# Kernel tuning notes

Hardware: AMD Instinct MI355X
Metric: run time of the kernel (lower is better)

The kernel has to match this reference:

```python
import jax, jax.numpy as jnp
import numpy as np

D_MODEL = 1024
NUM_HEADS = 16
HEAD_DIM = D_MODEL // NUM_HEADS  # 64
SEQ = 2048
BATCH = 4
LN_EPS = 1e-5


def setup_inputs() -> dict:
    key = jax.random.key(0)
    k_in, k_qkv, k_o, k_g = jax.random.split(key, 4)
    inputs = jax.random.normal(k_in, (BATCH, SEQ, D_MODEL), dtype=jnp.float32)
    mask = jnp.zeros((BATCH, 1, SEQ, SEQ), dtype=jnp.float32)  # additive mask
    # Realistic rotary embeddings (RoPE), duplicated-halves layout
    inv_freq = 1.0 / (10000.0 ** (jnp.arange(0, HEAD_DIM, 2, dtype=jnp.float32) / HEAD_DIM))
    pos = jnp.arange(SEQ, dtype=jnp.float32)
    freqs = pos[:, None] * inv_freq[None, :]            # [S, Dh/2]
    emb = jnp.concatenate([freqs, freqs], axis=-1)       # [S, Dh]
    cos = jnp.cos(emb)
    sin = jnp.sin(emb)
    # Parameters
    sd = 1.0 / np.sqrt(D_MODEL)
    w_qkv = jax.random.normal(k_qkv, (D_MODEL, 3 * D_MODEL), dtype=jnp.float32) * sd
    w_o = jax.random.normal(k_o, (D_MODEL, D_MODEL), dtype=jnp.float32) * sd
    ln_gamma = jnp.ones((D_MODEL,), dtype=jnp.float32)
    return {"inputs": inputs, "mask": mask, "cos": cos, "sin": sin,
            "ln_gamma": ln_gamma, "w_qkv": w_qkv, "w_o": w_o}


def _rotate_half(x):
    x1, x2 = jnp.split(x, 2, axis=-1)
    return jnp.concatenate([-x2, x1], axis=-1)


def reference(inputs, mask, cos, sin, ln_gamma, w_qkv, w_o):
    B, S, D = inputs.shape
    # Pre-attention LayerNorm (layer_id != 0), center=False -> no beta
    mu = jnp.mean(inputs, axis=-1, keepdims=True)
    var = jnp.mean(jnp.square(inputs - mu), axis=-1, keepdims=True)
    x = (inputs - mu) / jnp.sqrt(var + LN_EPS) * ln_gamma
    # Fused QKV projection, split into heads: [B, H, S, Dh]
    qkv = (x @ w_qkv).reshape(B, S, 3, NUM_HEADS, HEAD_DIM)
    qkv = jnp.transpose(qkv, (2, 0, 3, 1, 4))
    q, k, v = qkv[0], qkv[1], qkv[2]
    # RoPE
    c = cos.reshape(1, 1, S, HEAD_DIM)
    s = sin.reshape(1, 1, S, HEAD_DIM)
    q = q * c + _rotate_half(q) * s
    k = k * c + _rotate_half(k) * s
    # Scaled dot-product attention with additive mask
    scale = 1.0 / jnp.sqrt(jnp.asarray(HEAD_DIM, dtype=q.dtype))
    logits = jnp.einsum("bhqd,bhkd->bhqk", q, k) * scale + mask
    attn = jax.nn.softmax(logits, axis=-1)
    out = jnp.einsum("bhqk,bhkd->bhqd", attn, v)
    out = jnp.transpose(out, (0, 2, 1, 3)).reshape(B, S, D)
    return out @ w_o
```

## Files before the change

### kernel.cpp

```cpp
#include <hip/hip_runtime.h>
#include <stdint.h>

#define DEV __device__ __forceinline__

typedef __bf16 bf16x8 __attribute__((ext_vector_type(8)));
typedef float f32x4 __attribute__((ext_vector_type(4)));
typedef float f32x16 __attribute__((ext_vector_type(16)));

DEV unsigned short f2bf(float f) {
  union { float f; uint32_t u; } c; c.f = f;
  uint32_t u = c.u;
  u += 0x7FFFu + ((u >> 16) & 1u);
  return (unsigned short)(u >> 16);
}
DEV float bf2f(unsigned short h) {
  union { uint32_t u; float f; } c; c.u = ((uint32_t)h) << 16;
  return c.f;
}
DEV float u2f(uint32_t u) {
  union { uint32_t u; float f; } c; c.u = u;
  return c.f;
}
DEV bf16x8 ld8(const unsigned short* p) {
  uint4 u = *reinterpret_cast<const uint4*>(p);
  return __builtin_bit_cast(bf16x8, u);
}
DEV uint32_t cvtpk(float lo, float hi) {
  uint32_t r;
  asm("v_cvt_pk_bf16_f32 %0, %1, %2" : "=v"(r) : "v"(lo), "v"(hi));
  return r;
}
DEV void permswap(uint32_t& a, uint32_t& b) {
  asm("v_permlane32_swap_b32 %0, %1" : "+v"(a), "+v"(b));
}
DEV float exp2b(float x) { return __builtin_amdgcn_exp2f(x); }
DEV void gload16(const void* g, void* l) {
  __builtin_amdgcn_global_load_lds((const __attribute__((address_space(1))) void*)g,
                                   (__attribute__((address_space(3))) void*)l, 16, 0, 0);
}

template<int K, int N>
__global__ __launch_bounds__(256)
void transpose_cast_kernel(const float* __restrict__ in, unsigned short* __restrict__ out) {
  __shared__ float tile[64][65];
  const int bk = blockIdx.x % (K / 64);
  const int bn = blockIdx.x / (K / 64);
  const int k0 = bk * 64, n0 = bn * 64;
  const int t = threadIdx.x;
#pragma unroll
  for (int i = 0; i < 16; ++i) {
    int idx = t + i * 256;
    int kl = idx >> 6, nl = idx & 63;
    tile[kl][nl] = in[(size_t)(k0 + kl) * N + n0 + nl];
  }
  __syncthreads();
#pragma unroll
  for (int i = 0; i < 16; ++i) {
    int idx = t + i * 256;
    int nl = idx >> 6, kl = idx & 63;
    out[(size_t)(n0 + nl) * K + k0 + kl] = f2bf(tile[kl][nl]);
  }
}

__global__ __launch_bounds__(256)
void ln_kernel(const float* __restrict__ x, const float* __restrict__ gamma,
               unsigned short* __restrict__ y) {
  const int row = blockIdx.x;
  const int t = threadIdx.x;
  const float4 v = reinterpret_cast<const float4*>(x + (size_t)row * 1024)[t];
  float s  = v.x + v.y + v.z + v.w;
  float s2 = v.x * v.x + v.y * v.y + v.z * v.z + v.w * v.w;
#pragma unroll
  for (int off = 1; off < 64; off <<= 1) {
    s  += __shfl_xor(s, off);
    s2 += __shfl_xor(s2, off);
  }
  __shared__ float red[8];
  const int w = t >> 6, lane = t & 63;
  if (lane == 0) { red[w] = s; red[4 + w] = s2; }
  __syncthreads();
  s  = red[0] + red[1] + red[2] + red[3];
  s2 = red[4] + red[5] + red[6] + red[7];
  const float mu = s * (1.0f / 1024.0f);
  const float var = s2 * (1.0f / 1024.0f) - mu * mu;
  const float rstd = rsqrtf(var + 1e-5f);
  const float4 g = reinterpret_cast<const float4*>(gamma)[t];
  ushort4 o;
  o.x = f2bf((v.x - mu) * rstd * g.x);
  o.y = f2bf((v.y - mu) * rstd * g.y);
  o.z = f2bf((v.z - mu) * rstd * g.z);
  o.w = f2bf((v.w - mu) * rstd * g.w);
  reinterpret_cast<ushort4*>(y + (size_t)row * 1024)[t] = o;
}

template<int N_DIM>
__global__ __launch_bounds__(256)
void gemm_bt_kernel(const unsigned short* __restrict__ A,
                    const unsigned short* __restrict__ Bt,
                    float* __restrict__ Cout) {
  constexpr int K = 1024;
  __shared__ unsigned short a_lds[128 * 32];
  __shared__ unsigned short b_lds[128 * 32];
  const int t = threadIdx.x;
  const int w = t >> 6, l = t & 63;
  const int lrow = l & 15, lch = l >> 4;
  const int nbn = N_DIM / 128;
  const int m0 = (blockIdx.x / nbn) * 128;
  const int n0 = (blockIdx.x % nbn) * 128;
  const int wm = (w >> 1) * 64, wn = (w & 1) * 64;

  const int srow = t >> 2;
  const int schk = t & 3;
  const int scol = ((schk ^ (srow & 3)) << 3);
  const unsigned short* aS0 = A  + (size_t)(m0 + srow) * K + scol;
  const unsigned short* aS1 = A  + (size_t)(m0 + 64 + srow) * K + scol;
  const unsigned short* bS0 = Bt + (size_t)(n0 + srow) * K + scol;
  const unsigned short* bS1 = Bt + (size_t)(n0 + 64 + srow) * K + scol;
  unsigned short* aD0 = a_lds + (w * 16) * 32;
  unsigned short* aD1 = a_lds + (64 + w * 16) * 32;
  unsigned short* bD0 = b_lds + (w * 16) * 32;
  unsigned short* bD1 = b_lds + (64 + w * 16) * 32;

  f32x4 acc[4][4] = {};

  for (int k0 = 0; k0 < K; k0 += 32) {
    gload16(aS0 + k0, aD0);
    gload16(aS1 + k0, aD1);
    gload16(bS0 + k0, bD0);
    gload16(bS1 + k0, bD1);
    __syncthreads();
    bf16x8 af[4], bfr[4];
#pragma unroll
    for (int m = 0; m < 4; ++m) {
      int row = wm + m * 16 + lrow;
      af[m] = ld8(a_lds + row * 32 + ((lch ^ (lrow & 3)) << 3));
    }
#pragma unroll
    for (int n = 0; n < 4; ++n) {
      int row = wn + n * 16 + lrow;
      bfr[n] = ld8(b_lds + row * 32 + ((lch ^ (lrow & 3)) << 3));
    }
#pragma unroll
    for (int m = 0; m < 4; ++m)
#pragma unroll
      for (int n = 0; n < 4; ++n)
        acc[m][n] = __builtin_amdgcn_mfma_f32_16x16x32_bf16(af[m], bfr[n], acc[m][n], 0, 0, 0);
    __syncthreads();
  }

#pragma unroll
  for (int m = 0; m < 4; ++m) {
    const int grow0 = m0 + wm + m * 16 + lch * 4;
#pragma unroll
    for (int n = 0; n < 4; ++n) {
      const int gcol = n0 + wn + n * 16 + lrow;
#pragma unroll
      for (int r = 0; r < 4; ++r)
        Cout[(size_t)(grow0 + r) * N_DIM + gcol] = acc[m][n][r];
    }
  }
}

__global__ __launch_bounds__(256)
void gemm_qkv_rope_kernel(const unsigned short* __restrict__ A,
                          const unsigned short* __restrict__ Bt,
                          const float* __restrict__ cosb,
                          const float* __restrict__ sinb,
                          unsigned short* __restrict__ Qo,
                          unsigned short* __restrict__ Ko,
                          unsigned short* __restrict__ Vo) {
  constexpr int K = 1024;
  constexpr int N_DIM = 3072;
  __shared__ unsigned short a_lds[128 * 32];
  __shared__ unsigned short b_lds[128 * 32];
  const int t = threadIdx.x;
  const int w = t >> 6, l = t & 63;
  const int lrow = l & 15, lch = l >> 4;
  const int nbn = N_DIM / 128;
  const int m0 = (blockIdx.x / nbn) * 128;
  const int n0 = (blockIdx.x % nbn) * 128;
  const int wm = (w >> 1) * 64, wn = (w & 1) * 64;

  const int srow = t >> 2;
  const int schk = t & 3;
  const int scol = ((schk ^ (srow & 3)) << 3);
  const unsigned short* aS0 = A  + (size_t)(m0 + srow) * K + scol;
  const unsigned short* aS1 = A  + (size_t)(m0 + 64 + srow) * K + scol;
  const unsigned short* bS0 = Bt + (size_t)(n0 + srow) * K + scol;
  const unsigned short* bS1 = Bt + (size_t)(n0 + 64 + srow) * K + scol;
  unsigned short* aD0 = a_lds + (w * 16) * 32;
  unsigned short* aD1 = a_lds + (64 + w * 16) * 32;
  unsigned short* bD0 = b_lds + (w * 16) * 32;
  unsigned short* bD1 = b_lds + (64 + w * 16) * 32;

  f32x4 acc[4][4] = {};

  for (int k0 = 0; k0 < K; k0 += 32) {
    gload16(aS0 + k0, aD0);
    gload16(aS1 + k0, aD1);
    gload16(bS0 + k0, bD0);
    gload16(bS1 + k0, bD1);
    __syncthreads();
    bf16x8 af[4], bfr[4];
#pragma unroll
    for (int m = 0; m < 4; ++m) {
      int row = wm + m * 16 + lrow;
      af[m] = ld8(a_lds + row * 32 + ((lch ^ (lrow & 3)) << 3));
    }
#pragma unroll
    for (int n = 0; n < 4; ++n) {
      int row = wn + n * 16 + lrow;
      bfr[n] = ld8(b_lds + row * 32 + ((lch ^ (lrow & 3)) << 3));
    }
#pragma unroll
    for (int m = 0; m < 4; ++m)
#pragma unroll
      for (int n = 0; n < 4; ++n)
        acc[m][n] = __builtin_amdgcn_mfma_f32_16x16x32_bf16(af[m], bfr[n], acc[m][n], 0, 0, 0);
    __syncthreads();
  }

  const int b = m0 >> 11;
  const int sbase = (m0 & 2047) + wm;
  const int region = n0 >> 10;
  const int h = ((n0 & 1023) >> 6) + (w & 1);

  if (region < 2) {
    const float qs = (region == 0) ? 0.180336880f : 1.0f;
    unsigned short* dst = (region == 0 ? Qo : Ko) + (size_t)(b * 16 + h) * 2048 * 64;
#pragma unroll
    for (int m = 0; m < 4; ++m) {
#pragma unroll
      for (int r = 0; r < 4; ++r) {
        const int sg = sbase + m * 16 + lch * 4 + r;
        const float* crow = cosb + (size_t)sg * 64;
        const float* srow2 = sinb + (size_t)sg * 64;
        unsigned short* drow = dst + (size_t)sg * 64;
#pragma unroll
        for (int np = 0; np < 2; ++np) {
          const int d0 = np * 16 + lrow;
          const int d1 = d0 + 32;
          const float v0 = acc[m][np][r];
          const float v1 = acc[m][np + 2][r];
          const float r0 = v0 * crow[d0] - v1 * srow2[d0];
          const float r1 = v1 * crow[d1] + v0 * srow2[d1];
          drow[d0] = f2bf(r0 * qs);
          drow[d1] = f2bf(r1 * qs);
        }
      }
    }
  } else {
    unsigned short* dst = Vo + (size_t)(b * 16 + h) * 64 * 2048;
#pragma unroll
    for (int m = 0; m < 4; ++m) {
      const int sg0 = sbase + m * 16 + lch * 4;
#pragma unroll
      for (int np = 0; np < 4; ++np) {
        const int d = np * 16 + lrow;
        alignas(8) unsigned short o4[4];
#pragma unroll
        for (int r = 0; r < 4; ++r) o4[r] = f2bf(acc[m][np][r]);
        *(ushort4*)(dst + (size_t)d * 2048 + sg0) = *(ushort4*)o4;
      }
    }
  }
}

__global__ __launch_bounds__(256)
void mask_flags_kernel(const float* __restrict__ mask, unsigned char* __restrict__ flg) {
  const int bid = blockIdx.x;
  const int kvt = bid & 31, qc = (bid >> 5) & 31, b = bid >> 10;
  const int t = threadIdx.x;
  uint32_t orbits = 0;
  const int r = t >> 2, c0 = (t & 3) * 16;
  const float* src = mask + (size_t)b * (2048ull * 2048) + (size_t)(qc * 64 + r) * 2048 + kvt * 64 + c0;
#pragma unroll
  for (int i = 0; i < 4; ++i) {
    const float4 v = *(const float4*)(src + i * 4);
    orbits |= __float_as_uint(v.x) | __float_as_uint(v.y) |
              __float_as_uint(v.z) | __float_as_uint(v.w);
  }
  const int nz = __syncthreads_or(orbits != 0u);
  if (t == 0) flg[(size_t)(b * 32 + kvt) * 32 + qc] = (unsigned char)(nz != 0);
}

__global__ __launch_bounds__(256)
void mask_retile_kernel(const float* __restrict__ mask, unsigned short* __restrict__ mrs,
                        const unsigned char* __restrict__ flg) {
  const int bid = blockIdx.x;
  const int kvt = bid & 31, qc = (bid >> 5) & 31, b = bid >> 10;
  if (!flg[(size_t)(b * 32 + kvt) * 32 + qc]) return;
  const int t = threadIdx.x;
  __shared__ float tile[64][72];
  {
    const int r = t >> 2, c0 = (t & 3) * 16;
    const float* src = mask + (size_t)b * (2048ull * 2048) + (size_t)(qc * 64 + r) * 2048 + kvt * 64 + c0;
#pragma unroll
    for (int i = 0; i < 4; ++i) {
      const float4 v = *(const float4*)(src + i * 4);
      *(float4*)&tile[r][c0 + i * 4] = v;
    }
  }
  __syncthreads();
  const int cid = t >> 5;
  const int n = cid >> 2, jj = (cid >> 1) & 1, hi = cid & 1;
  const int qq0 = (t & 31) * 2;
  const int cb = n * 32 + jj * 16 + hi * 4;
  unsigned short* dst = mrs + (((size_t)(b * 32 + kvt) * 8 + cid) * 2048 + qc * 64) * 8;
#pragma unroll
  for (int qo = 0; qo < 2; ++qo) {
    const int q = qq0 + qo;
    alignas(16) unsigned short o8[8];
#pragma unroll
    for (int v = 0; v < 8; ++v) {
      const int col = cb + (v >> 2) * 8 + (v & 3);
      o8[v] = f2bf(tile[q][col] * 1.44269504f);
    }
    *(uint4*)(dst + (size_t)q * 8) = *(uint4*)o8;
  }
}

__global__ __launch_bounds__(256)
void attn_kernel(const unsigned short* __restrict__ Q,
                 const unsigned short* __restrict__ Kg,
                 const unsigned short* __restrict__ Vt,
                 const unsigned short* __restrict__ mrs,
                 const unsigned char* __restrict__ flg,
                 unsigned short* __restrict__ O) {
  const int t = threadIdx.x, w = t >> 6, l = t & 63;
  const int lq = l & 31, hi = l >> 5;
  const int bid = blockIdx.x;
  const int x = bid & 7, y = bid >> 3;
  const int bh = x * 8 + (y & 7), qb = y >> 3;
  const int b = bh >> 4, h = bh & 15;
  const int q0 = qb * 128 + w * 32;

  const unsigned short* Qb = Q  + (size_t)bh * (2048 * 64);
  const unsigned short* Kb = Kg + (size_t)bh * (2048 * 64);
  const unsigned short* Vb = Vt + (size_t)bh * (64 * 2048);
  const unsigned short* ml = mrs + (size_t)b * 4194304 + (size_t)hi * 16384 + (size_t)(q0 + lq) * 8;
  const unsigned char* fb = flg + (size_t)(b * 32) * 32 + qb * 2;

  __shared__ unsigned short k_lds[2][64 * 64];
  __shared__ unsigned short v_lds[2][64 * 64];

  bf16x8 qf[4];
  {
    const unsigned short* qp = Qb + (size_t)(q0 + lq) * 64 + hi * 8;
#pragma unroll
    for (int c = 0; c < 4; ++c) qf[c] = ld8(qp + c * 16);
  }
  bf16x8 ones;
  {
    const uint4 ou = { 0x3F803F80u, 0x3F803F80u, 0x3F803F80u, 0x3F803F80u };
    ones = __builtin_bit_cast(bf16x8, ou);
  }

  const int srow = t >> 2, sl0 = (t & 3) * 2, sl1 = sl0 + 1;
  const unsigned short* ks = Kb + (size_t)srow * 64 + sl0 * 8;
  const unsigned short* vs = Vb + (size_t)srow * 2048 + sl0 * 8;
  const int wd0 = srow * 64 + ((sl0 ^ (srow & 7)) << 3);
  const int wd1 = srow * 64 + ((sl1 ^ (srow & 7)) << 3);

  uint4 ka0 = *(const uint4*)ks;
  uint4 ka1 = *(const uint4*)(ks + 8);
  uint4 va0 = *(const uint4*)vs;
  uint4 va1 = *(const uint4*)(vs + 8);
  *(uint4*)(k_lds[0] + wd0) = ka0;
  *(uint4*)(k_lds[0] + wd1) = ka1;
  *(uint4*)(v_lds[0] + wd0) = va0;
  *(uint4*)(v_lds[0] + wd1) = va1;

  f32x16 ot0 = {}, ot1 = {};
  f32x16 st_sum = {};
  int cur = 0;
  const int lsw = lq & 7;

  uint4 mA[4], mB[4];

  auto do_tile = [&](int kv0, uint4 (&mcur)[4], uint4 (&mnext)[4],
                     bool hm, bool hmn) {
    __syncthreads();
    const bool more = (kv0 + 64) < 2048;
    if (more) {
      ka0 = *(const uint4*)(ks + (size_t)(kv0 + 64) * 64);
      ka1 = *(const uint4*)(ks + (size_t)(kv0 + 64) * 64 + 8);
      va0 = *(const uint4*)(vs + kv0 + 64);
      va1 = *(const uint4*)(vs + kv0 + 64 + 8);
      if (hmn) {
        const unsigned short* mp = ml + (size_t)(kv0 + 64) * 2048;
#pragma unroll
        for (int c2 = 0; c2 < 4; ++c2) mnext[c2] = *(const uint4*)(mp + c2 * 32768);
      }
    }

    f32x16 st0 = {}, st1 = {};
    if (hm) {
#pragma unroll
      for (int jj = 0; jj < 2; ++jj) {
        const uint4 u0 = mcur[jj];
        const uint4 u1 = mcur[2 + jj];
#pragma unroll
        for (int wv = 0; wv < 4; ++wv) {
          const uint32_t w0 = ((const uint32_t*)&u0)[wv];
          const uint32_t w1 = ((const uint32_t*)&u1)[wv];
          st0[jj * 8 + wv * 2]     = u2f(w0 << 16);
          st0[jj * 8 + wv * 2 + 1] = u2f(w0 & 0xffff0000u);
          st1[jj * 8 + wv * 2]     = u2f(w1 << 16);
          st1[jj * 8 + wv * 2 + 1] = u2f(w1 & 0xffff0000u);
        }
      }
    }

    const unsigned short* kb = k_lds[cur];
    __builtin_amdgcn_s_setprio(1);
#pragma unroll
    for (int c = 0; c < 4; ++c) {
      const int so = (((2 * c + hi) ^ lsw) << 3);
      const bf16x8 kf0 = ld8(kb + lq * 64 + so);
      const bf16x8 kf1 = ld8(kb + (32 + lq) * 64 + so);
      st0 = __builtin_amdgcn_mfma_f32_32x32x16_bf16(kf0, qf[c], st0, 0, 0, 0);
      st1 = __builtin_amdgcn_mfma_f32_32x32x16_bf16(kf1, qf[c], st1, 0, 0, 0);
    }
    __builtin_amdgcn_s_setprio(0);

#pragma unroll
    for (int r = 0; r < 16; ++r) {
      st0[r] = exp2b(st0[r]);
      st1[r] = exp2b(st1[r]);
    }

    bf16x8 pa[4];
#pragma unroll
    for (int c = 0; c < 4; ++c) {
      const int e8 = (c & 1) * 8;
      uint32_t A01, B01, A23, B23;
      if (c < 2) {
        A01 = cvtpk(st0[e8 + 0], st0[e8 + 1]);
        B01 = cvtpk(st0[e8 + 4], st0[e8 + 5]);
        A23 = cvtpk(st0[e8 + 2], st0[e8 + 3]);
        B23 = cvtpk(st0[e8 + 6], st0[e8 + 7]);
      } else {
        A01 = cvtpk(st1[e8 + 0], st1[e8 + 1]);
        B01 = cvtpk(st1[e8 + 4], st1[e8 + 5]);
        A23 = cvtpk(st1[e8 + 2], st1[e8 + 3]);
        B23 = cvtpk(st1[e8 + 6], st1[e8 + 7]);
      }
      permswap(A01, B01);
      permswap(A23, B23);
      const uint4 pw = { A01, A23, B01, B23 };
      pa[c] = __builtin_bit_cast(bf16x8, pw);
    }

    if (more) {
      unsigned short* kn = k_lds[cur ^ 1];
      unsigned short* vn = v_lds[cur ^ 1];
      *(uint4*)(kn + wd0) = ka0;
      *(uint4*)(kn + wd1) = ka1;
      *(uint4*)(vn + wd0) = va0;
      *(uint4*)(vn + wd1) = va1;
    }

    const unsigned short* vb = v_lds[cur];
    __builtin_amdgcn_s_setprio(1);
#pragma unroll
    for (int c = 0; c < 4; ++c) {
      const int so = (((2 * c + hi) ^ lsw) << 3);
      const bf16x8 vf0 = ld8(vb + lq * 64 + so);
      const bf16x8 vf1 = ld8(vb + (32 + lq) * 64 + so);
      ot0 = __builtin_amdgcn_mfma_f32_32x32x16_bf16(vf0, pa[c], ot0, 0, 0, 0);
      ot1 = __builtin_amdgcn_mfma_f32_32x32x16_bf16(vf1, pa[c], ot1, 0, 0, 0);
      st_sum = __builtin_amdgcn_mfma_f32_32x32x16_bf16(ones, pa[c], st_sum, 0, 0, 0);
    }
    __builtin_amdgcn_s_setprio(0);
    cur ^= 1;
  };

  unsigned int bm = 0;
  for (int kvt = 0; kvt < 32; ++kvt) bm |= fb[kvt * 32] | fb[kvt * 32 + 1];

  if (bm == 0) {
    for (int kv0 = 0; kv0 < 2048; kv0 += 128) {
      do_tile(kv0, mA, mB, false, false);
      do_tile(kv0 + 64, mB, mA, false, false);
    }
  } else {
    bool hmA = (fb[0] | fb[1]) != 0;
    if (hmA) {
#pragma unroll
      for (int c2 = 0; c2 < 4; ++c2) mA[c2] = *(const uint4*)(ml + c2 * 32768);
    }
    bool hmB = false;
    for (int kv0 = 0; kv0 < 2048; kv0 += 128) {
      const int tB = (kv0 >> 6) + 1;
      hmB = (kv0 + 64 < 2048) && ((fb[tB * 32] | fb[tB * 32 + 1]) != 0);
      do_tile(kv0, mA, mB, hmA, hmB);
      const int tA = tB + 1;
      hmA = (kv0 + 128 < 2048) && ((fb[tA * 32] | fb[tA * 32 + 1]) != 0);
      do_tile(kv0 + 64, mB, mA, hmB, hmA);
    }
  }

  const float inv = 1.0f / st_sum[0];
  unsigned short* ob = O + ((size_t)(b * 2048 + q0 + lq) * 16 + h) * 64 + hi * 4;
#pragma unroll
  for (int td = 0; td < 2; ++td) {
#pragma unroll
    for (int rr = 0; rr < 4; ++rr) {
      ushort4 ov;
      if (td == 0) {
        ov.x = f2bf(ot0[rr * 4 + 0] * inv);
        ov.y = f2bf(ot0[rr * 4 + 1] * inv);
        ov.z = f2bf(ot0[rr * 4 + 2] * inv);
        ov.w = f2bf(ot0[rr * 4 + 3] * inv);
      } else {
        ov.x = f2bf(ot1[rr * 4 + 0] * inv);
        ov.y = f2bf(ot1[rr * 4 + 1] * inv);
        ov.z = f2bf(ot1[rr * 4 + 2] * inv);
        ov.w = f2bf(ot1[rr * 4 + 3] * inv);
      }
      *(ushort4*)(ob + td * 32 + rr * 8) = ov;
    }
  }
}

extern "C" void kernel_launch(void* const* d_in, const int* in_sizes, int n_in,
                              void* d_out, int out_size, void* d_ws, size_t ws_size,
                              hipStream_t stream) {
  (void)in_sizes; (void)n_in; (void)out_size; (void)ws_size;
  const float* x     = (const float*)d_in[0];
  const float* mask  = (const float*)d_in[1];
  const float* cosb  = (const float*)d_in[2];
  const float* sinb  = (const float*)d_in[3];
  const float* gamma = (const float*)d_in[4];
  const float* w_qkv = (const float*)d_in[5];
  const float* w_o   = (const float*)d_in[6];

  char* ws = (char*)d_ws;
  unsigned short* x_bf   = (unsigned short*)(ws);
  unsigned short* wqkvT  = (unsigned short*)(ws + 16777216);
  unsigned short* woT    = (unsigned short*)(ws + 23068672);
  unsigned short* mask_rs = (unsigned short*)(ws + 25165824);
  unsigned char*  flags   = (unsigned char*)(ws + 25165824 + 33554432);
  unsigned short* q_r    = (unsigned short*)(ws + 75497472);
  unsigned short* k_r    = (unsigned short*)(ws + 92274688);
  unsigned short* v_t    = (unsigned short*)(ws + 109051904);
  unsigned short* attn   = (unsigned short*)(ws + 125829120);

  transpose_cast_kernel<1024, 3072><<<dim3(16 * 48), dim3(256), 0, stream>>>(w_qkv, wqkvT);
  transpose_cast_kernel<1024, 1024><<<dim3(16 * 16), dim3(256), 0, stream>>>(w_o, woT);
  ln_kernel<<<dim3(8192), dim3(256), 0, stream>>>(x, gamma, x_bf);
  gemm_qkv_rope_kernel<<<dim3(64 * 24), dim3(256), 0, stream>>>(x_bf, wqkvT, cosb, sinb, q_r, k_r, v_t);
  mask_flags_kernel<<<dim3(4096), dim3(256), 0, stream>>>(mask, flags);
  mask_retile_kernel<<<dim3(4096), dim3(256), 0, stream>>>(mask, mask_rs, flags);
  attn_kernel<<<dim3(1024), dim3(256), 0, stream>>>(q_r, k_r, v_t, mask_rs, flags, attn);
  gemm_bt_kernel<1024><<<dim3(64 * 8), dim3(256), 0, stream>>>(attn, woT, (float*)d_out);
}
```

Before: 233.2 us.

## Fuse mask flag and retile kernels; remap GEMM block IDs across XCDs

Merges the mask flag scan and the mask retile into one kernel, so the mask is read from global memory once and one launch is dropped. Remaps block indices in both GEMMs so that consecutive blocks landing on the same XCD (blockIdx mod 8) cover contiguous tiles, aiming for better L2 reuse of A and B tiles. The remap assumes the grid size is divisible by 8 and that hardware dispatches blocks round-robin across 8 XCDs.

```diff
diff --git a/kernel.cpp b/kernel.cpp
--- a/kernel.cpp
+++ b/kernel.cpp
@@ -99,14 +99,15 @@
                     const unsigned short* __restrict__ Bt,
                     float* __restrict__ Cout) {
   constexpr int K = 1024;
+  constexpr int nbn = N_DIM / 128;
   __shared__ unsigned short a_lds[128 * 32];
   __shared__ unsigned short b_lds[128 * 32];
   const int t = threadIdx.x;
   const int w = t >> 6, l = t & 63;
   const int lrow = l & 15, lch = l >> 4;
-  const int nbn = N_DIM / 128;
-  const int m0 = (blockIdx.x / nbn) * 128;
-  const int n0 = (blockIdx.x % nbn) * 128;
+  const int rid = (blockIdx.x & 7) * (8 * nbn) + (blockIdx.x >> 3);
+  const int m0 = (rid / nbn) * 128;
+  const int n0 = (rid % nbn) * 128;
   const int wm = (w >> 1) * 64, wn = (w & 1) * 64;
 
   const int srow = t >> 2;
@@ -170,16 +171,16 @@
                           unsigned short* __restrict__ Ko,
                           unsigned short* __restrict__ Vo) {
   constexpr int K = 1024;
-  constexpr int N_DIM = 3072;
+  constexpr int nbn = 24;
   __shared__ unsigned short a_lds[128 * 32];
   __shared__ unsigned short b_lds[128 * 32];
   const int t = threadIdx.x;
   const int w = t >> 6, l = t & 63;
   const int lrow = l & 15, lch = l >> 4;
-  const int nbn = N_DIM / 128;
-  const int m0 = (blockIdx.x / nbn) * 128;
-  const int n0 = (blockIdx.x % nbn) * 128;
-  const int wm = (w >> 1) * 64, wn = (w & 1) * 64;
+  const int rid = (blockIdx.x & 7) * 192 + (blockIdx.x >> 3);
+  const int m0 = (rid / nbn) * 128;
+  const int n0 = (rid % nbn) * 128;
+  const int wm = (w >> 1) * 64;
 
   const int srow = t >> 2;
   const int schk = t & 3;
@@ -209,7 +210,7 @@
     }
 #pragma unroll
     for (int n = 0; n < 4; ++n) {
-      int row = wn + n * 16 + lrow;
+      int row = (w & 1) * 64 + n * 16 + lrow;
       bfr[n] = ld8(b_lds + row * 32 + ((lch ^ (lrow & 3)) << 3));
     }
 #pragma unroll
@@ -267,40 +268,28 @@
 }
 
 __global__ __launch_bounds__(256)
-void mask_flags_kernel(const float* __restrict__ mask, unsigned char* __restrict__ flg) {
+void mask_prep_kernel(const float* __restrict__ mask, unsigned short* __restrict__ mrs,
+                      unsigned char* __restrict__ flg) {
   const int bid = blockIdx.x;
   const int kvt = bid & 31, qc = (bid >> 5) & 31, b = bid >> 10;
   const int t = threadIdx.x;
-  uint32_t orbits = 0;
   const int r = t >> 2, c0 = (t & 3) * 16;
   const float* src = mask + (size_t)b * (2048ull * 2048) + (size_t)(qc * 64 + r) * 2048 + kvt * 64 + c0;
+  float4 v4[4];
+  uint32_t orbits = 0;
 #pragma unroll
   for (int i = 0; i < 4; ++i) {
-    const float4 v = *(const float4*)(src + i * 4);
-    orbits |= __float_as_uint(v.x) | __float_as_uint(v.y) |
-              __float_as_uint(v.z) | __float_as_uint(v.w);
+    v4[i] = *(const float4*)(src + i * 4);
+    orbits |= __float_as_uint(v4[i].x) | __float_as_uint(v4[i].y) |
+              __float_as_uint(v4[i].z) | __float_as_uint(v4[i].w);
   }
   const int nz = __syncthreads_or(orbits != 0u);
   if (t == 0) flg[(size_t)(b * 32 + kvt) * 32 + qc] = (unsigned char)(nz != 0);
-}
-
-__global__ __launch_bounds__(256)
-void mask_retile_kernel(const float* __restrict__ mask, unsigned short* __restrict__ mrs,
-                        const unsigned char* __restrict__ flg) {
-  const int bid = blockIdx.x;
-  const int kvt = bid & 31, qc = (bid >> 5) & 31, b = bid >> 10;
-  if (!flg[(size_t)(b * 32 + kvt) * 32 + qc]) return;
-  const int t = threadIdx.x;
+  if (!nz) return;
+
   __shared__ float tile[64][72];
-  {
-    const int r = t >> 2, c0 = (t & 3) * 16;
-    const float* src = mask + (size_t)b * (2048ull * 2048) + (size_t)(qc * 64 + r) * 2048 + kvt * 64 + c0;
-#pragma unroll
-    for (int i = 0; i < 4; ++i) {
-      const float4 v = *(const float4*)(src + i * 4);
-      *(float4*)&tile[r][c0 + i * 4] = v;
-    }
-  }
+#pragma unroll
+  for (int i = 0; i < 4; ++i) *(float4*)&tile[r][c0 + i * 4] = v4[i];
   __syncthreads();
   const int cid = t >> 5;
   const int n = cid >> 2, jj = (cid >> 1) & 1, hi = cid & 1;
@@ -551,8 +540,7 @@
   transpose_cast_kernel<1024, 1024><<<dim3(16 * 16), dim3(256), 0, stream>>>(w_o, woT);
   ln_kernel<<<dim3(8192), dim3(256), 0, stream>>>(x, gamma, x_bf);
   gemm_qkv_rope_kernel<<<dim3(64 * 24), dim3(256), 0, stream>>>(x_bf, wqkvT, cosb, sinb, q_r, k_r, v_t);
-  mask_flags_kernel<<<dim3(4096), dim3(256), 0, stream>>>(mask, flags);
-  mask_retile_kernel<<<dim3(4096), dim3(256), 0, stream>>>(mask, mask_rs, flags);
+  mask_prep_kernel<<<dim3(4096), dim3(256), 0, stream>>>(mask, mask_rs, flags);
   attn_kernel<<<dim3(1024), dim3(256), 0, stream>>>(q_r, k_r, v_t, mask_rs, flags, attn);
   gemm_bt_kernel<1024><<<dim3(64 * 8), dim3(256), 0, stream>>>(attn, woT, (float*)d_out);
 }
```

After: 230.4 us. About the same (-1.2%).
